# Performance work log

Hardware: AMD Instinct MI355X
Metric: run time of the kernel (lower is better)

## Reference

```python
import jax, jax.numpy as jnp
import numpy as np

N, E, D, H, L, G, OUT = 16384, 65536, 64, 128, 3, 512, 128
EPS = 1e-5


def setup_inputs() -> dict:
    key = jax.random.key(0)
    ks = jax.random.split(key, 12)
    s = 0.05  # small init to keep res+ stack stable
    return {
        "x": jax.random.normal(ks[0], (N, D), jnp.float32),
        "edge_index": jax.random.randint(ks[1], (2, E), 0, N, jnp.int32),
        "edge_attr": jax.random.normal(ks[2], (E, D), jnp.float32),
        "batch": jnp.sort(jax.random.randint(ks[3], (N,), 0, G, jnp.int32)),
        # per-layer params, stacked on leading layer dim L
        "ln_scale": jnp.ones((L, D), jnp.float32),
        "ln_bias": jnp.zeros((L, D), jnp.float32),
        "W1": jax.random.normal(ks[4], (L, D, H), jnp.float32) * s,
        "b1": jnp.zeros((L, H), jnp.float32),
        "W2": jax.random.normal(ks[5], (L, H, D * D), jnp.float32) * s,
        "b2": jnp.zeros((L, D * D), jnp.float32),
        "root": jax.random.normal(ks[6], (L, D, D), jnp.float32) * s,
        "conv_b": jnp.zeros((L, D), jnp.float32),
        # head params
        "dense_W": jax.random.normal(ks[7], (D, D), jnp.float32) * s,
        "dense_b": jnp.zeros((D,), jnp.float32),
        "out_W": jax.random.normal(ks[8], (D, OUT), jnp.float32) * s,
        "out_b": jnp.zeros((OUT,), jnp.float32),
    }


def _layer_norm(h, scale, bias):
    mu = jnp.mean(h, axis=-1, keepdims=True)
    var = jnp.mean((h - mu) ** 2, axis=-1, keepdims=True)
    return (h - mu) * jax.lax.rsqrt(var + EPS) * scale + bias


def _gnn_layer(x, edge_index, edge_attr, ln_scale, ln_bias, W1, b1, W2, b2, root, conv_b):
    # DeepGCNLayer block='res+': h = conv(dropout(act(norm(x)))); return x + h
    # (dropout is identity in eval/reference)
    h = jax.nn.leaky_relu(_layer_norm(x, ln_scale, ln_bias))
    src, dst = edge_index[0], edge_index[1]
    # NNConv: per-edge DxD weight from edge MLP (MapE2NxN with LeakyReLU)
    w = jax.nn.leaky_relu(edge_attr @ W1 + b1) @ W2 + b2       # [E, D*D]
    w = w.reshape(-1, D, D)                                     # [E, D, D]
    msg = jnp.einsum('ed,edf->ef', h[src], w)                   # [E, D]
    num = jax.ops.segment_sum(msg, dst, num_segments=N)         # [N, D]
    deg = jax.ops.segment_sum(jnp.ones((msg.shape[0],), msg.dtype), dst, num_segments=N)
    agg = num / jnp.maximum(deg, 1.0)[:, None]                  # mean aggregation
    conv = agg + h @ root + conv_b                              # root weight + bias
    return x + conv


def reference(x, edge_index, edge_attr, batch, ln_scale, ln_bias, W1, b1, W2, b2,
              root, conv_b, dense_W, dense_b, out_W, out_b):
    for l in range(L):
        x = _gnn_layer(x, edge_index, edge_attr, ln_scale[l], ln_bias[l],
                       W1[l], b1[l], W2[l], b2[l], root[l], conv_b[l])
    x = x @ dense_W + dense_b
    # global_mean_pool over graphs
    num = jax.ops.segment_sum(x, batch, num_segments=G)
    cnt = jax.ops.segment_sum(jnp.ones((x.shape[0],), x.dtype), batch, num_segments=G)
    pooled = num / jnp.maximum(cnt, 1.0)[:, None]
    pooled = jax.nn.leaky_relu(pooled)
    return pooled @ out_W + out_b
```

## Files before the change

kernel.cpp:

```cpp
#include <hip/hip_runtime.h>
#include <hip/hip_bf16.h>

#define NN 16384
#define EE 65536
#define DD 64
#define HH 128
#define LL 3
#define GG 512
#define OUTD 128
#define NEG 0.01f

#define CHUNK 8192
#define KSEG 8


typedef __attribute__((ext_vector_type(8))) short short8;
typedef __attribute__((ext_vector_type(4))) float f32x4;

__device__ __forceinline__ float leaky(float x){ return x > 0.f ? x : NEG * x; }
__device__ __forceinline__ unsigned short f2bf(float f){
  union { float f; unsigned int u; } v; v.f = f;
  unsigned int r = v.u + 0x7fffu + ((v.u >> 16) & 1u);
  return (unsigned short)(r >> 16);
}

#define CV_A (EE*DD)
#define CV_B (LL*HH*DD)
#define CV_C (LL*64*8192)
#define PRE0 (NN/4)
#define PRE1 ((CV_A+CV_B+CV_C)/256)
#define PRE2 (EE/256)

__global__ void k_pre(const float* x_in, const float* ln_s, const float* ln_b,
                      float* x_cur, float* h, int* deg, int* cursor, int* cnt, float* pooled,
                      const float* ea, const float* W1, const float* W2,
                      unsigned short* eab, unsigned short* W1T, unsigned short* W2T,
                      const int* ei, const int* batch){
  int t = threadIdx.x;
  int b = blockIdx.x;
  if (b < PRE0){
    int i = b*256 + t;
    if (i < NN){ deg[i] = 0; cursor[i] = 0; }
    if (i < GG) cnt[i] = 0;
    if (i < GG*DD) pooled[i] = 0.f;
    int lane = t & 63, nl = t >> 6;
    int n = b*4 + nl;
    float v = x_in[(size_t)n*DD + lane];
    x_cur[(size_t)n*DD + lane] = v;
    float s = v;
    for (int m=1;m<64;m<<=1) s += __shfl_xor(s, m, 64);
    float mu = s * (1.0f/64.0f);
    float dv = v - mu;
    float q = dv*dv;
    for (int m=1;m<64;m<<=1) q += __shfl_xor(q, m, 64);
    float var = q * (1.0f/64.0f);
    float w = dv * rsqrtf(var + 1e-5f) * ln_s[lane] + ln_b[lane];
    h[(size_t)n*DD + lane] = leaky(w);
    return;
  }
  if (b < PRE0 + PRE1){
    int idx = (b - PRE0)*256 + t;
    if (idx < CV_A){
      eab[idx] = f2bf(ea[idx]);
    } else if (idx < CV_A + CV_B){
      int i = idx - CV_A;
      int l = i >> 13, r = i & 8191;
      int j = r >> 6, d = r & 63;
      W1T[i] = f2bf(W1[(size_t)l*DD*HH + d*HH + j]);
    } else {
      int i = idx - CV_A - CV_B;
      int l = i >> 19, rem = i & ((1<<19)-1);
      int f = rem >> 13, c = rem & 8191;
      int kk = c & 1, j = (c>>1) & 3, lane = (c>>3) & 63, ii = (c>>9) & 7, q = (c>>12) & 1;
      int idxu = 2*lane + kk;
      int d = 32*q + 4*ii + j;
      int kd = idxu*64 + d;
      W2T[i] = f2bf(W2[(size_t)l*HH*DD*DD + (size_t)kd*DD + f]);
    }
    return;
  }
  {
    int e = (b - PRE0 - PRE1)*256 + t;
    atomicAdd(&deg[ei[EE + e]], 1);
    if (e < NN) atomicAdd(&cnt[batch[e]], 1);
  }
}

__global__ void k_scan(const int* deg, int* row_ptr){
  __shared__ int part[256];
  int t = threadIdx.x;
  int base = t*64; int s = 0;
  for (int i=0;i<64;++i) s += deg[base+i];
  part[t] = s; __syncthreads();
  for (int off=1; off<256; off<<=1){
    int v = (t>=off)?part[t-off]:0; __syncthreads();
    part[t] += v; __syncthreads();
  }
  int run = (t==0)?0:part[t-1];
  if (t==0) row_ptr[0] = 0;
  for (int i=0;i<64;++i){ run += deg[base+i]; row_ptr[base+i+1] = run; }
}
__global__ void k_fill(const int* ei, const int* row_ptr, int* cursor,
                       int* edge_id, int* src_sorted){
  int e = blockIdx.x*256 + threadIdx.x;
  if (e < EE){
    int d = ei[EE + e];
    int pos = row_ptr[d] + atomicAdd(&cursor[d], 1);
    edge_id[pos] = e;
    src_sorted[pos] = ei[e];
  }
}

__global__ __launch_bounds__(256, 2)
void k_mlp3(const unsigned short* eab, const unsigned short* W1T, const float* b1,
            unsigned short* ug){
  __shared__ __align__(16) unsigned short a_lds[128][72];
  __shared__ __align__(16) unsigned short b_lds[128][72];
  __shared__ __align__(16) unsigned short c_lds[128][136];
  int t = threadIdx.x;
  int l  = blockIdx.x >> 9;
  int e0 = (blockIdx.x & 511) * 128;
  {
    int row = t >> 1, col = (t & 1) * 32;
    const float4* sa = (const float4*)(eab + (size_t)(e0 + row)*DD + col);
    const float4* sb = (const float4*)(W1T + (size_t)l*HH*DD + (size_t)row*DD + col);
    #pragma unroll
    for (int i=0;i<4;++i){
      *(float4*)&a_lds[row][col + 8*i] = sa[i];
      *(float4*)&b_lds[row][col + 8*i] = sb[i];
    }
  }
  __syncthreads();
  int wave = t >> 6, lane = t & 63;
  int m0 = (wave >> 1) * 64, j0 = (wave & 1) * 64;
  int lr = lane & 15, lq = lane >> 4;
  f32x4 acc[4][4];
  #pragma unroll
  for (int a=0;a<4;++a)
    #pragma unroll
    for (int b=0;b<4;++b) acc[a][b] = (f32x4){0.f,0.f,0.f,0.f};
  #pragma unroll
  for (int ks=0; ks<2; ++ks){
    short8 av[4];
    #pragma unroll
    for (int mt=0; mt<4; ++mt) av[mt] = *(const short8*)&a_lds[m0 + mt*16 + lr][ks*32 + lq*8];
    #pragma unroll
    for (int jt=0; jt<4; ++jt){
      short8 bv = *(const short8*)&b_lds[j0 + jt*16 + lr][ks*32 + lq*8];
      #pragma unroll
      for (int mt=0; mt<4; ++mt)
        acc[mt][jt] = __builtin_amdgcn_mfma_f32_16x16x32_bf16(av[mt], bv, acc[mt][jt], 0, 0, 0);
    }
  }
  #pragma unroll
  for (int mt=0; mt<4; ++mt)
    #pragma unroll
    for (int jt=0; jt<4; ++jt){
      int col = j0 + jt*16 + lr;
      float bj = b1[l*HH + col];
      #pragma unroll
      for (int r=0; r<4; ++r){
        int row = m0 + mt*16 + lq*4 + r;
        c_lds[row][col] = f2bf(leaky(acc[mt][jt][r] + bj));
      }
    }
  __syncthreads();
  {
    int row = t >> 1, half = t & 1;
    float4* dst = (float4*)(ug + (size_t)l*EE*HH + (size_t)(e0 + row)*HH + half*64);
    #pragma unroll
    for (int i=0;i<8;++i) dst[i] = *(const float4*)&c_lds[row][half*64 + 8*i];
  }
}

__global__ __launch_bounds__(256, 4)
void k_sbuild4(const unsigned short* ug, const float* h, const int* row_ptr,
               const int* edge_id, const int* src_sorted,
               unsigned short* S, float* Hs, int chunk_base){
  int t = threadIdx.x, wave = t >> 6, lane = t & 63;
  int q = wave & 1;
  int nloc = blockIdx.x*2 + (wave >> 1);
  int n = chunk_base + nloc;
  int r0 = row_ptr[n], r1 = row_ptr[n+1];
  int dbase = 32*q;
  int lhalf = lane & 31;
  const unsigned int* ugd = (const unsigned int*)ug;
  float acc[64];
  #pragma unroll
  for (int i=0;i<64;++i) acc[i] = 0.f;
  float hs = 0.f;
  int pos = r0;
  for (; pos + 4 <= r1; pos += 4){
    int ea0 = edge_id[pos],    eb0 = edge_id[pos+1];
    int ea1 = edge_id[pos+2],  eb1 = edge_id[pos+3];
    int sa0 = src_sorted[pos],   sb0 = src_sorted[pos+1];
    int sa1 = src_sorted[pos+2], sb1 = src_sorted[pos+3];
    int sel0 = (lane < 32) ? sa0 : sb0;
    int sel1 = (lane < 32) ? sa1 : sb1;
    float hv0 = h[(size_t)sel0*DD + dbase + lhalf];
    float hv1 = h[(size_t)sel1*DD + dbase + lhalf];
    unsigned int ua0 = ugd[(size_t)ea0*64 + lane];
    unsigned int ub0 = ugd[(size_t)eb0*64 + lane];
    unsigned int ua1 = ugd[(size_t)ea1*64 + lane];
    unsigned int ub1 = ugd[(size_t)eb1*64 + lane];
    hs += hv0 + hv1;
    int h0 = __float_as_int(hv0), h1 = __float_as_int(hv1);
    float ua0l = __uint_as_float(ua0 << 16), ua0h = __uint_as_float(ua0 & 0xFFFF0000u);
    float ub0l = __uint_as_float(ub0 << 16), ub0h = __uint_as_float(ub0 & 0xFFFF0000u);
    float ua1l = __uint_as_float(ua1 << 16), ua1h = __uint_as_float(ua1 & 0xFFFF0000u);
    float ub1l = __uint_as_float(ub1 << 16), ub1h = __uint_as_float(ub1 & 0xFFFF0000u);
    #pragma unroll
    for (int dd=0; dd<32; ++dd){
      float sa_ = __int_as_float(__builtin_amdgcn_readlane(h0, dd));
      float sb_ = __int_as_float(__builtin_amdgcn_readlane(h0, 32+dd));
      float sa2 = __int_as_float(__builtin_amdgcn_readlane(h1, dd));
      float sb2 = __int_as_float(__builtin_amdgcn_readlane(h1, 32+dd));
      acc[dd*2+0] += ua0l*sa_; acc[dd*2+1] += ua0h*sa_;
      acc[dd*2+0] += ub0l*sb_; acc[dd*2+1] += ub0h*sb_;
      acc[dd*2+0] += ua1l*sa2; acc[dd*2+1] += ua1h*sa2;
      acc[dd*2+0] += ub1l*sb2; acc[dd*2+1] += ub1h*sb2;
    }
  }
  for (; pos + 2 <= r1; pos += 2){
    int ea = edge_id[pos],  eb = edge_id[pos+1];
    int sa = src_sorted[pos], sb = src_sorted[pos+1];
    int sel = (lane < 32) ? sa : sb;
    float hv = h[(size_t)sel*DD + dbase + lhalf];
    unsigned int ua = ugd[(size_t)ea*64 + lane];
    unsigned int ub = ugd[(size_t)eb*64 + lane];
    hs += hv;
    int h0 = __float_as_int(hv);
    float ual = __uint_as_float(ua << 16), uah = __uint_as_float(ua & 0xFFFF0000u);
    float ubl = __uint_as_float(ub << 16), ubh = __uint_as_float(ub & 0xFFFF0000u);
    #pragma unroll
    for (int dd=0; dd<32; ++dd){
      float sa_ = __int_as_float(__builtin_amdgcn_readlane(h0, dd));
      float sb_ = __int_as_float(__builtin_amdgcn_readlane(h0, 32+dd));
      acc[dd*2+0] += ual*sa_; acc[dd*2+1] += uah*sa_;
      acc[dd*2+0] += ubl*sb_; acc[dd*2+1] += ubh*sb_;
    }
  }
  if (pos < r1){
    int e = edge_id[pos], s = src_sorted[pos];
    float hv = h[(size_t)s*DD + dbase + lhalf];
    unsigned int ua = ugd[(size_t)e*64 + lane];
    hs += (lane < 32) ? hv : 0.f;
    int h0 = __float_as_int(hv);
    float ual = __uint_as_float(ua << 16), uah = __uint_as_float(ua & 0xFFFF0000u);
    #pragma unroll
    for (int dd=0; dd<32; ++dd){
      float sa_ = __int_as_float(__builtin_amdgcn_readlane(h0, dd));
      acc[dd*2+0] += ual*sa_; acc[dd*2+1] += uah*sa_;
    }
  }
  float4* Srow4 = (float4*)(S + (size_t)nloc*8192);
  #pragma unroll
  for (int i=0;i<8;++i){
    union { unsigned int u[4]; float4 v; } b;
    #pragma unroll
    for (int j=0;j<4;++j){
      int dd = 4*i + j;
      b.u[j] = (unsigned int)f2bf(acc[dd*2+0]) | ((unsigned int)f2bf(acc[dd*2+1]) << 16);
    }
    Srow4[(q*8 + i)*64 + lane] = b.v;
  }
  float hs2 = hs + __shfl_xor(hs, 32, 64);
  if (lane < 32) Hs[(size_t)n*DD + dbase + lane] = hs2;
}

__global__ __launch_bounds__(256, 2)
void k_gemm(const unsigned short* S, const unsigned short* W2T,
            float* num_part, int chunk_base){
  __shared__ __align__(16) unsigned short a_lds[128][136];
  __shared__ __align__(16) unsigned short b_lds[64][136];
  int t = threadIdx.x;
  int wave = t >> 6, lane = t & 63;
  int rowblk = blockIdx.x, kseg = blockIdx.y;
  int lr = lane & 15, lq = lane >> 4;
  f32x4 acc[2][4];
  #pragma unroll
  for (int a=0;a<2;++a)
    #pragma unroll
    for (int b=0;b<4;++b) acc[a][b] = (f32x4){0.f,0.f,0.f,0.f};
  int m0 = wave * 32;
  int ra = t >> 1, qa = t & 1;
  int rb = t >> 2, qb = t & 3;
  for (int it = 0; it < 8; ++it){
    int kbase = kseg*1024 + it*128;
    {
      const float4* sa = (const float4*)(S + (size_t)(rowblk*128 + ra)*8192 + kbase + qa*64);
      float4* da = (float4*)&a_lds[ra][qa*64];
      #pragma unroll
      for (int i=0;i<8;++i) da[i] = sa[i];
      const float4* sb = (const float4*)(W2T + (size_t)rb*8192 + kbase + qb*32);
      float4* db = (float4*)&b_lds[rb][qb*32];
      #pragma unroll
      for (int i=0;i<4;++i) db[i] = sb[i];
    }
    __syncthreads();
    #pragma unroll
    for (int kk=0; kk<128; kk+=32){
      short8 a0 = *(const short8*)&a_lds[m0 + lr][kk + lq*8];
      short8 a1 = *(const short8*)&a_lds[m0 + 16 + lr][kk + lq*8];
      #pragma unroll
      for (int ft=0; ft<4; ++ft){
        short8 bv = *(const short8*)&b_lds[ft*16 + lr][kk + lq*8];
        acc[0][ft] = __builtin_amdgcn_mfma_f32_16x16x32_bf16(a0, bv, acc[0][ft], 0, 0, 0);
        acc[1][ft] = __builtin_amdgcn_mfma_f32_16x16x32_bf16(a1, bv, acc[1][ft], 0, 0, 0);
      }
    }
    __syncthreads();
  }
  float* dstp = num_part + (size_t)kseg*NN*DD;
  #pragma unroll
  for (int rt=0; rt<2; ++rt)
    #pragma unroll
    for (int ft=0; ft<4; ++ft)
      #pragma unroll
      for (int rr=0; rr<4; ++rr){
        int m = m0 + rt*16 + lq*4 + rr;
        int f = ft*16 + lr;
        int n = chunk_base + rowblk*128 + m;
        dstp[(size_t)n*DD + f] = acc[rt][ft][rr];
      }
}

__global__ void k_update_ln(float* x, const float* num_part, float* h, const float* Hs,
                            const int* deg, const float* root, const float* b2,
                            const float* conv_b, const float* ln_s, const float* ln_b,
                            int l, int do_ln){
  __shared__ float rl[64][64];
  __shared__ float b2l[64][64];
  __shared__ float hrow[4][64];
  __shared__ float hsrow[4][64];
  int t = threadIdx.x;
  int f = t & 63, nl = t >> 6;
  for (int idx=t; idx<4096; idx+=256){
    rl[idx>>6][idx&63]  = root[(size_t)l*4096 + idx];
    b2l[idx>>6][idx&63] = b2[(size_t)l*4096 + idx];
  }
  int n = blockIdx.x*4 + nl;
  hrow[nl][f]  = h[(size_t)n*DD + f];
  hsrow[nl][f] = Hs[(size_t)n*DD + f];
  __syncthreads();
  float dg = (float)deg[n]; if (dg < 1.f) dg = 1.f;
  float nsum = 0.f;
  #pragma unroll
  for (int p=0; p<KSEG; ++p) nsum += num_part[(size_t)p*NN*DD + (size_t)n*DD + f];
  float acc = x[(size_t)n*DD + f] + nsum/dg + conv_b[l*DD + f];
  #pragma unroll
  for (int d=0; d<64; ++d)
    acc += hrow[nl][d]*rl[d][f] + hsrow[nl][d]*b2l[d][f];
  x[(size_t)n*DD + f] = acc;
  if (do_ln){
    int lp = l + 1;
    float s = acc;
    for (int m=1;m<64;m<<=1) s += __shfl_xor(s, m, 64);
    float mu = s * (1.0f/64.0f);
    float dv = acc - mu;
    float qv = dv*dv;
    for (int m=1;m<64;m<<=1) qv += __shfl_xor(qv, m, 64);
    float var = qv * (1.0f/64.0f);
    float w = dv * rsqrtf(var + 1e-5f) * ln_s[lp*DD + f] + ln_b[lp*DD + f];
    h[(size_t)n*DD + f] = leaky(w);
  }
}

__global__ void k_dense_pool(const float* x, const float* dW, const float* db,
                             const int* batch, float* pooled){
  __shared__ float wl[64][64];
  __shared__ float xrow[4][64];
  int t = threadIdx.x;
  int f = t & 63, nl = t >> 6;
  for (int idx=t; idx<4096; idx+=256) wl[idx>>6][idx&63] = dW[idx];
  int n = blockIdx.x*4 + nl;
  xrow[nl][f] = x[(size_t)n*DD + f];
  __syncthreads();
  float acc = db[f];
  #pragma unroll
  for (int d=0; d<64; ++d) acc += xrow[nl][d]*wl[d][f];
  atomicAdd(&pooled[(size_t)batch[n]*DD + f], acc);
}

__global__ void k_final(const float* pooled, const int* cnt, const float* oW,
                        const float* ob, float* out){
  __shared__ float p[64];
  int g = blockIdx.x, t = threadIdx.x;
  if (t < 64){
    float c = (float)cnt[g]; if (c < 1.f) c = 1.f;
    p[t] = leaky(pooled[(size_t)g*DD + t] / c);
  }
  __syncthreads();
  float acc = ob[t];
  #pragma unroll
  for (int f=0; f<64; ++f) acc += p[f]*oW[(size_t)f*OUTD + t];
  out[(size_t)g*OUTD + t] = acc;
}

__global__ void k_diag(float* out, float val, int n){
  int i = blockIdx.x*256 + threadIdx.x;
  if (i < n) out[i] = (i==0) ? val : 0.f;
}

extern "C" void kernel_launch(void* const* d_in, const int* in_sizes, int n_in,
                              void* d_out, int out_size, void* d_ws, size_t ws_size,
                              hipStream_t stream){
  const float* x_in  = (const float*)d_in[0];
  const int*   ei    = (const int*)d_in[1];
  const float* ea    = (const float*)d_in[2];
  const int*   batch = (const int*)d_in[3];
  const float* ln_s  = (const float*)d_in[4];
  const float* ln_b  = (const float*)d_in[5];
  const float* W1    = (const float*)d_in[6];
  const float* b1    = (const float*)d_in[7];
  const float* W2    = (const float*)d_in[8];
  const float* b2    = (const float*)d_in[9];
  const float* root  = (const float*)d_in[10];
  const float* convb = (const float*)d_in[11];
  const float* dW    = (const float*)d_in[12];
  const float* db    = (const float*)d_in[13];
  const float* oW    = (const float*)d_in[14];
  const float* ob    = (const float*)d_in[15];
  float* out = (float*)d_out;

  char* ws = (char*)d_ws;
  size_t off = 0;
  auto alloc = [&](size_t bytes)->char*{
    char* p = ws + off; off = (off + bytes + 255) & ~(size_t)255; return p;
  };
  float* x_cur  = (float*)alloc((size_t)NN*DD*4);
  float* h      = (float*)alloc((size_t)NN*DD*4);
  unsigned short* ug  = (unsigned short*)alloc((size_t)LL*EE*HH*2);
  float* num_part = (float*)alloc((size_t)KSEG*NN*DD*4);
  float* Hs     = (float*)alloc((size_t)NN*DD*4);
  unsigned short* S   = (unsigned short*)alloc((size_t)CHUNK*8192*2);
  unsigned short* W2T = (unsigned short*)alloc((size_t)LL*8192*64*2);
  unsigned short* eab = (unsigned short*)alloc((size_t)EE*DD*2);
  unsigned short* W1T = (unsigned short*)alloc((size_t)LL*HH*DD*2);
  int* deg     = (int*)alloc((size_t)NN*4);
  int* row_ptr = (int*)alloc((size_t)(NN+1)*4);
  int* cursor  = (int*)alloc((size_t)NN*4);
  int* edge_id = (int*)alloc((size_t)EE*4);
  int* src_sorted = (int*)alloc((size_t)EE*4);
  int* cnt     = (int*)alloc((size_t)GG*4);
  float* pooled= (float*)alloc((size_t)GG*DD*4);
  size_t needed = off;
  if (ws_size < needed){
    k_diag<<<(out_size+255)/256, 256, 0, stream>>>(out, (float)ws_size, out_size);
    return;
  }

  k_pre <<<PRE0+PRE1+PRE2, 256, 0, stream>>>(x_in, ln_s, ln_b, x_cur, h, deg, cursor, cnt,
                                             pooled, ea, W1, W2, eab, W1T, W2T, ei, batch);
  k_scan<<<1, 256, 0, stream>>>(deg, row_ptr);
  k_fill<<<EE/256, 256, 0, stream>>>(ei, row_ptr, cursor, edge_id, src_sorted);
  k_mlp3<<<LL*(EE/128), 256, 0, stream>>>(eab, W1T, b1, ug);

  for (int l=0; l<LL; ++l){
    const unsigned short* ugl = ug + (size_t)l*EE*HH;
    for (int c=0; c<NN/CHUNK; ++c){
      k_sbuild4<<<CHUNK/2, 256, 0, stream>>>(ugl, h, row_ptr, edge_id, src_sorted, S, Hs, c*CHUNK);
      k_gemm   <<<dim3(CHUNK/128, KSEG), 256, 0, stream>>>(S, W2T + (size_t)l*8192*64, num_part, c*CHUNK);
    }
    k_update_ln<<<NN/4, 256, 0, stream>>>(x_cur, num_part, h, Hs, deg, root, b2, convb,
                                          ln_s, ln_b, l, (l < LL-1) ? 1 : 0);
  }
  k_dense_pool<<<NN/4, 256, 0, stream>>>(x_cur, dW, db, batch, pooled);
  k_final     <<<GG, 128, 0, stream>>>(pooled, cnt, oW, ob, out);
}
```

Measured before the change: 604.2 us.

## Overlap edge S-build with previous chunk's GEMM in one fused launch

```diff
diff --git a/kernel.cpp b/kernel.cpp
--- a/kernel.cpp
+++ b/kernel.cpp
@@ -10,8 +10,10 @@
 #define OUTD 128
 #define NEG 0.01f
 
-#define CHUNK 8192
+#define CHUNK 4096
 #define KSEG 8
+#define SBB (CHUNK/2)
+#define GMB ((CHUNK/128)*KSEG)
 
 
 typedef __attribute__((ext_vector_type(8))) short short8;
@@ -173,171 +175,178 @@
   }
 }
 
-__global__ __launch_bounds__(256, 4)
-void k_sbuild4(const unsigned short* ug, const float* h, const int* row_ptr,
-               const int* edge_id, const int* src_sorted,
-               unsigned short* S, float* Hs, int chunk_base){
+__global__ __launch_bounds__(256, 2)
+void k_sbgm(const unsigned short* ug, const float* h, const int* row_ptr,
+            const int* edge_id, const int* src_sorted,
+            unsigned short* S_w, float* Hs, int sb_base, int sb_blocks,
+            const unsigned short* S_r, const unsigned short* W2T,
+            float* num_part, int gm_base){
+  __shared__ __align__(16) unsigned short a_lds[128][72];
+  __shared__ __align__(16) unsigned short b_lds[64][72];
   int t = threadIdx.x, wave = t >> 6, lane = t & 63;
-  int q = wave & 1;
-  int nloc = blockIdx.x*2 + (wave >> 1);
-  int n = chunk_base + nloc;
-  int r0 = row_ptr[n], r1 = row_ptr[n+1];
-  int dbase = 32*q;
-  int lhalf = lane & 31;
-  const unsigned int* ugd = (const unsigned int*)ug;
-  float acc[64];
-  #pragma unroll
-  for (int i=0;i<64;++i) acc[i] = 0.f;
-  float hs = 0.f;
-  int pos = r0;
-  for (; pos + 4 <= r1; pos += 4){
-    int ea0 = edge_id[pos],    eb0 = edge_id[pos+1];
-    int ea1 = edge_id[pos+2],  eb1 = edge_id[pos+3];
-    int sa0 = src_sorted[pos],   sb0 = src_sorted[pos+1];
-    int sa1 = src_sorted[pos+2], sb1 = src_sorted[pos+3];
-    int sel0 = (lane < 32) ? sa0 : sb0;
-    int sel1 = (lane < 32) ? sa1 : sb1;
-    float hv0 = h[(size_t)sel0*DD + dbase + lhalf];
-    float hv1 = h[(size_t)sel1*DD + dbase + lhalf];
-    unsigned int ua0 = ugd[(size_t)ea0*64 + lane];
-    unsigned int ub0 = ugd[(size_t)eb0*64 + lane];
-    unsigned int ua1 = ugd[(size_t)ea1*64 + lane];
-    unsigned int ub1 = ugd[(size_t)eb1*64 + lane];
-    hs += hv0 + hv1;
-    int h0 = __float_as_int(hv0), h1 = __float_as_int(hv1);
-    float ua0l = __uint_as_float(ua0 << 16), ua0h = __uint_as_float(ua0 & 0xFFFF0000u);
-    float ub0l = __uint_as_float(ub0 << 16), ub0h = __uint_as_float(ub0 & 0xFFFF0000u);
-    float ua1l = __uint_as_float(ua1 << 16), ua1h = __uint_as_float(ua1 & 0xFFFF0000u);
-    float ub1l = __uint_as_float(ub1 << 16), ub1h = __uint_as_float(ub1 & 0xFFFF0000u);
-    #pragma unroll
-    for (int dd=0; dd<32; ++dd){
-      float sa_ = __int_as_float(__builtin_amdgcn_readlane(h0, dd));
-      float sb_ = __int_as_float(__builtin_amdgcn_readlane(h0, 32+dd));
-      float sa2 = __int_as_float(__builtin_amdgcn_readlane(h1, dd));
-      float sb2 = __int_as_float(__builtin_amdgcn_readlane(h1, 32+dd));
-      acc[dd*2+0] += ua0l*sa_; acc[dd*2+1] += ua0h*sa_;
-      acc[dd*2+0] += ub0l*sb_; acc[dd*2+1] += ub0h*sb_;
-      acc[dd*2+0] += ua1l*sa2; acc[dd*2+1] += ua1h*sa2;
-      acc[dd*2+0] += ub1l*sb2; acc[dd*2+1] += ub1h*sb2;
-    }
-  }
-  for (; pos + 2 <= r1; pos += 2){
-    int ea = edge_id[pos],  eb = edge_id[pos+1];
-    int sa = src_sorted[pos], sb = src_sorted[pos+1];
-    int sel = (lane < 32) ? sa : sb;
-    float hv = h[(size_t)sel*DD + dbase + lhalf];
-    unsigned int ua = ugd[(size_t)ea*64 + lane];
-    unsigned int ub = ugd[(size_t)eb*64 + lane];
-    hs += hv;
-    int h0 = __float_as_int(hv);
-    float ual = __uint_as_float(ua << 16), uah = __uint_as_float(ua & 0xFFFF0000u);
-    float ubl = __uint_as_float(ub << 16), ubh = __uint_as_float(ub & 0xFFFF0000u);
-    #pragma unroll
-    for (int dd=0; dd<32; ++dd){
-      float sa_ = __int_as_float(__builtin_amdgcn_readlane(h0, dd));
-      float sb_ = __int_as_float(__builtin_amdgcn_readlane(h0, 32+dd));
-      acc[dd*2+0] += ual*sa_; acc[dd*2+1] += uah*sa_;
-      acc[dd*2+0] += ubl*sb_; acc[dd*2+1] += ubh*sb_;
-    }
-  }
-  if (pos < r1){
-    int e = edge_id[pos], s = src_sorted[pos];
-    float hv = h[(size_t)s*DD + dbase + lhalf];
-    unsigned int ua = ugd[(size_t)e*64 + lane];
-    hs += (lane < 32) ? hv : 0.f;
-    int h0 = __float_as_int(hv);
-    float ual = __uint_as_float(ua << 16), uah = __uint_as_float(ua & 0xFFFF0000u);
-    #pragma unroll
-    for (int dd=0; dd<32; ++dd){
-      float sa_ = __int_as_float(__builtin_amdgcn_readlane(h0, dd));
-      acc[dd*2+0] += ual*sa_; acc[dd*2+1] += uah*sa_;
-    }
-  }
-  float4* Srow4 = (float4*)(S + (size_t)nloc*8192);
-  #pragma unroll
-  for (int i=0;i<8;++i){
-    union { unsigned int u[4]; float4 v; } b;
-    #pragma unroll
-    for (int j=0;j<4;++j){
-      int dd = 4*i + j;
-      b.u[j] = (unsigned int)f2bf(acc[dd*2+0]) | ((unsigned int)f2bf(acc[dd*2+1]) << 16);
-    }
-    Srow4[(q*8 + i)*64 + lane] = b.v;
-  }
-  float hs2 = hs + __shfl_xor(hs, 32, 64);
-  if (lane < 32) Hs[(size_t)n*DD + dbase + lane] = hs2;
-}
-
-__global__ __launch_bounds__(256, 2)
-void k_gemm(const unsigned short* S, const unsigned short* W2T,
-            float* num_part, int chunk_base){
-  __shared__ __align__(16) unsigned short a_lds[128][136];
-  __shared__ __align__(16) unsigned short b_lds[64][136];
-  int t = threadIdx.x;
-  int wave = t >> 6, lane = t & 63;
-  int rowblk = blockIdx.x, kseg = blockIdx.y;
-  int lr = lane & 15, lq = lane >> 4;
-  f32x4 acc[2][4];
-  #pragma unroll
-  for (int a=0;a<2;++a)
-    #pragma unroll
-    for (int b=0;b<4;++b) acc[a][b] = (f32x4){0.f,0.f,0.f,0.f};
-  int m0 = wave * 32;
-  int ra = t >> 1, qa = t & 1;
-  int rb = t >> 2, qb = t & 3;
-  for (int it = 0; it < 8; ++it){
-    int kbase = kseg*1024 + it*128;
-    {
-      const float4* sa = (const float4*)(S + (size_t)(rowblk*128 + ra)*8192 + kbase + qa*64);
-      float4* da = (float4*)&a_lds[ra][qa*64];
-      #pragma unroll
-      for (int i=0;i<8;++i) da[i] = sa[i];
-      const float4* sb = (const float4*)(W2T + (size_t)rb*8192 + kbase + qb*32);
-      float4* db = (float4*)&b_lds[rb][qb*32];
-      #pragma unroll
-      for (int i=0;i<4;++i) db[i] = sb[i];
-    }
-    __syncthreads();
-    #pragma unroll
-    for (int kk=0; kk<128; kk+=32){
-      short8 a0 = *(const short8*)&a_lds[m0 + lr][kk + lq*8];
-      short8 a1 = *(const short8*)&a_lds[m0 + 16 + lr][kk + lq*8];
-      #pragma unroll
-      for (int ft=0; ft<4; ++ft){
-        short8 bv = *(const short8*)&b_lds[ft*16 + lr][kk + lq*8];
-        acc[0][ft] = __builtin_amdgcn_mfma_f32_16x16x32_bf16(a0, bv, acc[0][ft], 0, 0, 0);
-        acc[1][ft] = __builtin_amdgcn_mfma_f32_16x16x32_bf16(a1, bv, acc[1][ft], 0, 0, 0);
-      }
-    }
-    __syncthreads();
-  }
-  float* dstp = num_part + (size_t)kseg*NN*DD;
-  #pragma unroll
-  for (int rt=0; rt<2; ++rt)
-    #pragma unroll
-    for (int ft=0; ft<4; ++ft)
-      #pragma unroll
-      for (int rr=0; rr<4; ++rr){
-        int m = m0 + rt*16 + lq*4 + rr;
-        int f = ft*16 + lr;
-        int n = chunk_base + rowblk*128 + m;
-        dstp[(size_t)n*DD + f] = acc[rt][ft][rr];
-      }
+  if ((int)blockIdx.x < sb_blocks){
+    int q = wave & 1;
+    int nloc = blockIdx.x*2 + (wave >> 1);
+    int n = sb_base + nloc;
+    int r0 = row_ptr[n], r1 = row_ptr[n+1];
+    int dbase = 32*q;
+    int lhalf = lane & 31;
+    const unsigned int* ugd = (const unsigned int*)ug;
+    float acc[64];
+    #pragma unroll
+    for (int i=0;i<64;++i) acc[i] = 0.f;
+    float hs = 0.f;
+    int pos = r0;
+    for (; pos + 4 <= r1; pos += 4){
+      int ea0 = edge_id[pos],    eb0 = edge_id[pos+1];
+      int ea1 = edge_id[pos+2],  eb1 = edge_id[pos+3];
+      int sa0 = src_sorted[pos],   sb0 = src_sorted[pos+1];
+      int sa1 = src_sorted[pos+2], sb1 = src_sorted[pos+3];
+      int sel0 = (lane < 32) ? sa0 : sb0;
+      int sel1 = (lane < 32) ? sa1 : sb1;
+      float hv0 = h[(size_t)sel0*DD + dbase + lhalf];
+      float hv1 = h[(size_t)sel1*DD + dbase + lhalf];
+      unsigned int ua0 = ugd[(size_t)ea0*64 + lane];
+      unsigned int ub0 = ugd[(size_t)eb0*64 + lane];
+      unsigned int ua1 = ugd[(size_t)ea1*64 + lane];
+      unsigned int ub1 = ugd[(size_t)eb1*64 + lane];
+      hs += hv0 + hv1;
+      int h0 = __float_as_int(hv0), h1 = __float_as_int(hv1);
+      float ua0l = __uint_as_float(ua0 << 16), ua0h = __uint_as_float(ua0 & 0xFFFF0000u);
+      float ub0l = __uint_as_float(ub0 << 16), ub0h = __uint_as_float(ub0 & 0xFFFF0000u);
+      float ua1l = __uint_as_float(ua1 << 16), ua1h = __uint_as_float(ua1 & 0xFFFF0000u);
+      float ub1l = __uint_as_float(ub1 << 16), ub1h = __uint_as_float(ub1 & 0xFFFF0000u);
+      #pragma unroll
+      for (int dd=0; dd<32; ++dd){
+        float sa_ = __int_as_float(__builtin_amdgcn_readlane(h0, dd));
+        float sb_ = __int_as_float(__builtin_amdgcn_readlane(h0, 32+dd));
+        float sa2 = __int_as_float(__builtin_amdgcn_readlane(h1, dd));
+        float sb2 = __int_as_float(__builtin_amdgcn_readlane(h1, 32+dd));
+        acc[dd*2+0] += ua0l*sa_; acc[dd*2+1] += ua0h*sa_;
+        acc[dd*2+0] += ub0l*sb_; acc[dd*2+1] += ub0h*sb_;
+        acc[dd*2+0] += ua1l*sa2; acc[dd*2+1] += ua1h*sa2;
+        acc[dd*2+0] += ub1l*sb2; acc[dd*2+1] += ub1h*sb2;
+      }
+    }
+    for (; pos + 2 <= r1; pos += 2){
+      int ea = edge_id[pos],  eb = edge_id[pos+1];
+      int sa = src_sorted[pos], sb = src_sorted[pos+1];
+      int sel = (lane < 32) ? sa : sb;
+      float hv = h[(size_t)sel*DD + dbase + lhalf];
+      unsigned int ua = ugd[(size_t)ea*64 + lane];
+      unsigned int ub = ugd[(size_t)eb*64 + lane];
+      hs += hv;
+      int h0 = __float_as_int(hv);
+      float ual = __uint_as_float(ua << 16), uah = __uint_as_float(ua & 0xFFFF0000u);
+      float ubl = __uint_as_float(ub << 16), ubh = __uint_as_float(ub & 0xFFFF0000u);
+      #pragma unroll
+      for (int dd=0; dd<32; ++dd){
+        float sa_ = __int_as_float(__builtin_amdgcn_readlane(h0, dd));
+        float sb_ = __int_as_float(__builtin_amdgcn_readlane(h0, 32+dd));
+        acc[dd*2+0] += ual*sa_; acc[dd*2+1] += uah*sa_;
+        acc[dd*2+0] += ubl*sb_; acc[dd*2+1] += ubh*sb_;
+      }
+    }
+    if (pos < r1){
+      int e = edge_id[pos], s = src_sorted[pos];
+      float hv = h[(size_t)s*DD + dbase + lhalf];
+      unsigned int ua = ugd[(size_t)e*64 + lane];
+      hs += (lane < 32) ? hv : 0.f;
+      int h0 = __float_as_int(hv);
+      float ual = __uint_as_float(ua << 16), uah = __uint_as_float(ua & 0xFFFF0000u);
+      #pragma unroll
+      for (int dd=0; dd<32; ++dd){
+        float sa_ = __int_as_float(__builtin_amdgcn_readlane(h0, dd));
+        acc[dd*2+0] += ual*sa_; acc[dd*2+1] += uah*sa_;
+      }
+    }
+    float4* Srow4 = (float4*)(S_w + (size_t)nloc*8192);
+    #pragma unroll
+    for (int i=0;i<8;++i){
+      union { unsigned int u[4]; float4 v; } b;
+      #pragma unroll
+      for (int j=0;j<4;++j){
+        int dd = 4*i + j;
+        b.u[j] = (unsigned int)f2bf(acc[dd*2+0]) | ((unsigned int)f2bf(acc[dd*2+1]) << 16);
+      }
+      Srow4[(q*8 + i)*64 + lane] = b.v;
+    }
+    float hs2 = hs + __shfl_xor(hs, 32, 64);
+    if (lane < 32) Hs[(size_t)n*DD + dbase + lane] = hs2;
+    return;
+  }
+  {
+    int g = blockIdx.x - sb_blocks;
+    int kseg = g & 7, rowblk = g >> 3;
+    int lr = lane & 15, lq = lane >> 4;
+    f32x4 acc[2][4];
+    #pragma unroll
+    for (int a=0;a<2;++a)
+      #pragma unroll
+      for (int b=0;b<4;++b) acc[a][b] = (f32x4){0.f,0.f,0.f,0.f};
+    int m0 = wave * 32;
+    for (int it = 0; it < 16; ++it){
+      int kbase = kseg*1024 + it*64;
+      #pragma unroll
+      for (int ii=0; ii<4; ++ii){
+        int idx = t + 256*ii;
+        int r = idx >> 3, c8 = (idx & 7) << 3;
+        *(float4*)&a_lds[r][c8] =
+          *(const float4*)(S_r + (size_t)(rowblk*128 + r)*8192 + kbase + c8);
+      }
+      #pragma unroll
+      for (int ii=0; ii<2; ++ii){
+        int idx = t + 256*ii;
+        int r = idx >> 3, c8 = (idx & 7) << 3;
+        *(float4*)&b_lds[r][c8] =
+          *(const float4*)(W2T + (size_t)r*8192 + kbase + c8);
+      }
+      __syncthreads();
+      #pragma unroll
+      for (int kk=0; kk<64; kk+=32){
+        short8 a0 = *(const short8*)&a_lds[m0 + lr][kk + lq*8];
+        short8 a1 = *(const short8*)&a_lds[m0 + 16 + lr][kk + lq*8];
+        #pragma unroll
+        for (int ft=0; ft<4; ++ft){
+          short8 bv = *(const short8*)&b_lds[ft*16 + lr][kk + lq*8];
+          acc[0][ft] = __builtin_amdgcn_mfma_f32_16x16x32_bf16(a0, bv, acc[0][ft], 0, 0, 0);
+          acc[1][ft] = __builtin_amdgcn_mfma_f32_16x16x32_bf16(a1, bv, acc[1][ft], 0, 0, 0);
+        }
+      }
+      __syncthreads();
+    }
+    float* dstp = num_part + (size_t)kseg*NN*DD;
+    #pragma unroll
+    for (int rt=0; rt<2; ++rt)
+      #pragma unroll
+      for (int ft=0; ft<4; ++ft)
+        #pragma unroll
+        for (int rr=0; rr<4; ++rr){
+          int m = m0 + rt*16 + lq*4 + rr;
+          int f = ft*16 + lr;
+          int n = gm_base + rowblk*128 + m;
+          dstp[(size_t)n*DD + f] = acc[rt][ft][rr];
+        }
+  }
 }
 
 __global__ void k_update_ln(float* x, const float* num_part, float* h, const float* Hs,
                             const int* deg, const float* root, const float* b2,
                             const float* conv_b, const float* ln_s, const float* ln_b,
-                            int l, int do_ln){
+                            const float* dW, const float* db, const int* batch, float* pooled,
+                            int l, int do_ln, int do_head){
   __shared__ float rl[64][64];
   __shared__ float b2l[64][64];
+  __shared__ float wl[64][64];
   __shared__ float hrow[4][64];
   __shared__ float hsrow[4][64];
+  __shared__ float xrow[4][64];
   int t = threadIdx.x;
   int f = t & 63, nl = t >> 6;
   for (int idx=t; idx<4096; idx+=256){
     rl[idx>>6][idx&63]  = root[(size_t)l*4096 + idx];
     b2l[idx>>6][idx&63] = b2[(size_t)l*4096 + idx];
+    if (do_head) wl[idx>>6][idx&63] = dW[idx];
   }
   int n = blockIdx.x*4 + nl;
   hrow[nl][f]  = h[(size_t)n*DD + f];
@@ -364,22 +373,14 @@
     float w = dv * rsqrtf(var + 1e-5f) * ln_s[lp*DD + f] + ln_b[lp*DD + f];
     h[(size_t)n*DD + f] = leaky(w);
   }
-}
-
-__global__ void k_dense_pool(const float* x, const float* dW, const float* db,
-                             const int* batch, float* pooled){
-  __shared__ float wl[64][64];
-  __shared__ float xrow[4][64];
-  int t = threadIdx.x;
-  int f = t & 63, nl = t >> 6;
-  for (int idx=t; idx<4096; idx+=256) wl[idx>>6][idx&63] = dW[idx];
-  int n = blockIdx.x*4 + nl;
-  xrow[nl][f] = x[(size_t)n*DD + f];
-  __syncthreads();
-  float acc = db[f];
-  #pragma unroll
-  for (int d=0; d<64; ++d) acc += xrow[nl][d]*wl[d][f];
-  atomicAdd(&pooled[(size_t)batch[n]*DD + f], acc);
+  if (do_head){
+    xrow[nl][f] = acc;
+    __syncthreads();
+    float hacc = db[f];
+    #pragma unroll
+    for (int d=0; d<64; ++d) hacc += xrow[nl][d]*wl[d][f];
+    atomicAdd(&pooled[(size_t)batch[n]*DD + f], hacc);
+  }
 }
 
 __global__ void k_final(const float* pooled, const int* cnt, const float* oW,
@@ -433,7 +434,8 @@
   unsigned short* ug  = (unsigned short*)alloc((size_t)LL*EE*HH*2);
   float* num_part = (float*)alloc((size_t)KSEG*NN*DD*4);
   float* Hs     = (float*)alloc((size_t)NN*DD*4);
-  unsigned short* S   = (unsigned short*)alloc((size_t)CHUNK*8192*2);
+  unsigned short* Sb0 = (unsigned short*)alloc((size_t)CHUNK*8192*2);
+  unsigned short* Sb1 = (unsigned short*)alloc((size_t)CHUNK*8192*2);
   unsigned short* W2T = (unsigned short*)alloc((size_t)LL*8192*64*2);
   unsigned short* eab = (unsigned short*)alloc((size_t)EE*DD*2);
   unsigned short* W1T = (unsigned short*)alloc((size_t)LL*HH*DD*2);
@@ -456,15 +458,22 @@
   k_fill<<<EE/256, 256, 0, stream>>>(ei, row_ptr, cursor, edge_id, src_sorted);
   k_mlp3<<<LL*(EE/128), 256, 0, stream>>>(eab, W1T, b1, ug);
 
+  unsigned short* Sb[2] = {Sb0, Sb1};
   for (int l=0; l<LL; ++l){
     const unsigned short* ugl = ug + (size_t)l*EE*HH;
-    for (int c=0; c<NN/CHUNK; ++c){
-      k_sbuild4<<<CHUNK/2, 256, 0, stream>>>(ugl, h, row_ptr, edge_id, src_sorted, S, Hs, c*CHUNK);
-      k_gemm   <<<dim3(CHUNK/128, KSEG), 256, 0, stream>>>(S, W2T + (size_t)l*8192*64, num_part, c*CHUNK);
-    }
+    const unsigned short* ks  = W2T + (size_t)l*8192*64;
+    k_sbgm<<<SBB, 256, 0, stream>>>(ugl, h, row_ptr, edge_id, src_sorted,
+                                    Sb[0], Hs, 0*CHUNK, SBB, Sb[1], ks, num_part, 0);
+    for (int c=1; c<4; ++c){
+      k_sbgm<<<SBB+GMB, 256, 0, stream>>>(ugl, h, row_ptr, edge_id, src_sorted,
+                                          Sb[c&1], Hs, c*CHUNK, SBB,
+                                          Sb[(c-1)&1], ks, num_part, (c-1)*CHUNK);
+    }
+    k_sbgm<<<GMB, 256, 0, stream>>>(ugl, h, row_ptr, edge_id, src_sorted,
+                                    Sb[0], Hs, 0, 0, Sb[1], ks, num_part, 3*CHUNK);
     k_update_ln<<<NN/4, 256, 0, stream>>>(x_cur, num_part, h, Hs, deg, root, b2, convb,
-                                          ln_s, ln_b, l, (l < LL-1) ? 1 : 0);
-  }
-  k_dense_pool<<<NN/4, 256, 0, stream>>>(x_cur, dW, db, batch, pooled);
-  k_final     <<<GG, 128, 0, stream>>>(pooled, cnt, oW, ob, out);
-}
+                                          ln_s, ln_b, dW, db, batch, pooled,
+                                          l, (l < LL-1) ? 1 : 0, (l == LL-1) ? 1 : 0);
+  }
+  k_final<<<GG, 128, 0, stream>>>(pooled, cnt, oW, ob, out);
+}
```

Result: slower. 723.9 us (+19.8%).
